# Optimization experiments

Hardware: AMD Instinct MI355X
Metric: run time of the kernel (lower is better)

The kernel has to match this reference:

```python
import jax, jax.numpy as jnp
import numpy as np

S, L, V, E, H, LBL, CH = 4096, 16, 100000, 256, 512, 64, 4


def setup_inputs() -> dict:
    key = jax.random.key(0)
    ks = jax.random.split(key, 10)
    sc = lambda k, shp, fan: (jax.random.normal(k, shp, jnp.float32) / np.sqrt(fan)).astype(jnp.float32)
    return {
        "sentence": jax.random.randint(ks[0], (S,), 0, V, dtype=jnp.int32),
        "chars": jax.random.normal(ks[1], (S, L), dtype=jnp.float32),
        "char_lens": jax.random.randint(ks[2], (S,), 1, L + 1, dtype=jnp.int32),
        "emb": jax.random.normal(ks[3], (V, E), dtype=jnp.float32),
        "W_ih_c": sc(ks[4], (4 * CH, 1), 1),
        "W_hh_c": sc(ks[5], (4 * CH, CH), CH),
        "b_ih_c": jnp.zeros((4 * CH,), jnp.float32),
        "b_hh_c": jnp.zeros((4 * CH,), jnp.float32),
        "W_ih_w": sc(ks[6], (4 * H, E + CH), E + CH),
        "W_hh_w": sc(ks[7], (4 * H, H), H),
        "b_ih_w": jnp.zeros((4 * H,), jnp.float32),
        "b_hh_w": jnp.zeros((4 * H,), jnp.float32),
        "W_out": sc(ks[8], (LBL, H), H),
        "b_out": jnp.zeros((LBL,), jnp.float32),
    }


def _lstm_gates(gates, c):
    i, f, g, o = jnp.split(gates, 4, axis=-1)
    c_new = jax.nn.sigmoid(f) * c + jax.nn.sigmoid(i) * jnp.tanh(g)
    h_new = jax.nn.sigmoid(o) * jnp.tanh(c_new)
    return h_new, c_new


def reference(sentence, chars, char_lens, emb, W_ih_c, W_hh_c, b_ih_c, b_hh_c,
              W_ih_w, W_hh_w, b_ih_w, b_hh_w, W_out, b_out):
    s, l = chars.shape
    # --- char-level LSTM, batched over all words (ragged -> padded + mask) ---
    # input projection: input_size == 1, so gates_x[s, t] = chars[s, t] * W_ih_c[:, 0] + b_ih_c
    gx = chars[:, :, None] * W_ih_c[:, 0] + b_ih_c          # [S, L, 4*CH]
    gx_t = jnp.transpose(gx, (1, 0, 2))                      # [L, S, 4*CH]
    mask = (jnp.arange(l)[:, None] < char_lens[None, :])[:, :, None]  # [L, S, 1]

    def char_step(carry, inp):
        h, c = carry
        g, m = inp
        h_new, c_new = _lstm_gates(g + h @ W_hh_c.T + b_hh_c, c)
        return (jnp.where(m, h_new, h), jnp.where(m, c_new, c)), None

    ch0 = jnp.zeros((s, W_hh_c.shape[1]), chars.dtype)
    (h_char, _), _ = jax.lax.scan(char_step, (ch0, ch0), (gx_t, mask))  # h_char: [S, CH]

    # --- word-level LSTM over the sentence ---
    word_in = jnp.concatenate([emb[sentence], h_char], axis=-1)  # [S, E+CH]
    gx_w = word_in @ W_ih_w.T + b_ih_w                           # [S, 4*H]

    def word_step(carry, g):
        h, c = carry
        h_new, c_new = _lstm_gates(g + h @ W_hh_w.T + b_hh_w, c)
        return (h_new, c_new), h_new

    wh0 = jnp.zeros((W_hh_w.shape[1],), chars.dtype)
    _, hs = jax.lax.scan(word_step, (wh0, wh0), gx_w)            # [S, H]

    logits = hs @ W_out.T + b_out                                # [S, LBL]
    return jax.nn.log_softmax(logits, axis=-1)
```

## Files before the change

kernel.cpp:

```cpp
#include <hip/hip_runtime.h>
#include <stdint.h>

#define SLEN 4096
#define CLEN 16
#define EDIM 256
#define HDIM 512
#define CHD  4
#define NLBL 64
#define KIN  260
#define G4H  2048

typedef unsigned long long u64;

__device__ __forceinline__ float sigf(float x){ return 1.0f/(1.0f+__expf(-x)); }
__device__ __forceinline__ float ftanh(float x){
  float e = __expf(2.0f*x);
  return 1.0f - 2.0f/(e+1.0f);
}
#define RLANE(x,i) __uint_as_float(__builtin_amdgcn_readlane(__float_as_uint(x),(i)))

__global__ void k_char_lstm(const float* __restrict__ chars, const int* __restrict__ lens,
                            const float* __restrict__ Wih, const float* __restrict__ Whh,
                            const float* __restrict__ bih, const float* __restrict__ bhh,
                            float* __restrict__ h_char){
  int s = blockIdx.x*blockDim.x + threadIdx.x;
  if (s >= SLEN) return;
  float wih[16], bb[16], whh[16][4];
  #pragma unroll
  for(int r=0;r<16;r++){
    wih[r]=Wih[r]; bb[r]=bih[r]+bhh[r];
    #pragma unroll
    for(int k=0;k<4;k++) whh[r][k]=Whh[r*4+k];
  }
  float x[16];
  #pragma unroll
  for(int i=0;i<4;i++){
    float4 v = *(const float4*)&chars[s*CLEN + 4*i];
    x[4*i+0]=v.x; x[4*i+1]=v.y; x[4*i+2]=v.z; x[4*i+3]=v.w;
  }
  float h[4]={0,0,0,0}, c[4]={0,0,0,0};
  int len = lens[s];
  #pragma unroll 1
  for(int t=0;t<CLEN;t++){
    float g[16];
    #pragma unroll
    for(int r=0;r<16;r++){
      float a = fmaf(x[t], wih[r], bb[r]);
      #pragma unroll
      for(int k=0;k<4;k++) a = fmaf(h[k], whh[r][k], a);
      g[r]=a;
    }
    bool m = t < len;
    #pragma unroll
    for(int j=0;j<4;j++){
      float ig=sigf(g[j]), fg=sigf(g[4+j]), gg=ftanh(g[8+j]), og=sigf(g[12+j]);
      float cn = fg*c[j] + ig*gg;
      float hn = og*ftanh(cn);
      if(m){ c[j]=cn; h[j]=hn; }
    }
  }
  #pragma unroll
  for(int j=0;j<4;j++) h_char[s*CHD+j]=h[j];
}

__global__ void k_gather(const int* __restrict__ sent, const float* __restrict__ emb,
                         const float* __restrict__ h_char, float* __restrict__ win){
  int s = blockIdx.x; int l = threadIdx.x;
  int row = sent[s];
  float4 v = *(const float4*)&emb[(size_t)row*EDIM + 4*l];
  *(float4*)&win[(size_t)s*KIN + 4*l] = v;
  if (l < CHD) win[(size_t)s*KIN + EDIM + l] = h_char[s*CHD + l];
}

#define BK 20
__global__ __launch_bounds__(256) void k_gemm_gx(const float* __restrict__ win,
                          const float* __restrict__ Wihw, float* __restrict__ gx){
  __shared__ float As[BK][68];
  __shared__ float Bs[BK][68];
  int s0 = blockIdx.x*64, n0 = blockIdx.y*64;
  int tid = threadIdx.x;
  int tm = tid>>4, tn = tid&15;
  float acc[4][4] = {};
  for(int k0=0;k0<KIN;k0+=BK){
    __syncthreads();
    #pragma unroll
    for(int i=0;i<5;i++){
      int e = tid + i*256;
      int m = e/BK, kk = e - m*BK;
      As[kk][m] = win[(size_t)(s0+m)*KIN + k0+kk];
      Bs[kk][m] = Wihw[(size_t)(n0+m)*KIN + k0+kk];
    }
    __syncthreads();
    #pragma unroll
    for(int kk=0;kk<BK;kk++){
      float4 a4 = *(const float4*)&As[kk][tm*4];
      float4 b4 = *(const float4*)&Bs[kk][tn*4];
      float av[4]={a4.x,a4.y,a4.z,a4.w};
      float bv[4]={b4.x,b4.y,b4.z,b4.w};
      #pragma unroll
      for(int i=0;i<4;i++)
        #pragma unroll
        for(int j=0;j<4;j++)
          acc[i][j] = fmaf(av[i], bv[j], acc[i][j]);
    }
  }
  #pragma unroll
  for(int i=0;i<4;i++){
    float4 o; o.x=acc[i][0]; o.y=acc[i][1]; o.z=acc[i][2]; o.w=acc[i][3];
    *(float4*)&gx[(size_t)(s0+tm*4+i)*G4H + n0 + tn*4] = o;
  }
}

__global__ __launch_bounds__(512) void k_word_lstm(const float* __restrict__ gx,
    const float* __restrict__ Whh, const float* __restrict__ bih, const float* __restrict__ bhh,
    u64* __restrict__ comm, float* __restrict__ hs){
  __shared__ float pbuf[2][8][64];
  const int tid = threadIdx.x;
  const int g   = blockIdx.x;
  const int w   = tid>>6;
  const int l   = tid&63;
  const int R   = (l>>4)*HDIM + g*16 + (l&15);
  const int gi  = g*16 + tid;
  float4 w4[16];
  #pragma unroll
  for(int i=0;i<16;i++) w4[i] = *(const float4*)&Whh[(size_t)R*HDIM + w*64 + 4*i];
  float cst = 0.f;
  float bsum[4], gxv[4];
  if (tid<16){
    #pragma unroll
    for(int q=0;q<4;q++){
      bsum[q] = bih[q*HDIM + gi] + bhh[q*HDIM + gi];
      gxv[q]  = gx[(size_t)0*G4H + q*HDIM + gi];
    }
  }

  #pragma unroll 1
  for(int t=0;t<SLEN;t++){
    const int par = t&1;
    float hv = 0.f;
    if (t>0){
      const u64* slot = &comm[(size_t)par*HDIM + w*64 + l];
      u64 v;
      do { v = __hip_atomic_load(slot, __ATOMIC_RELAXED, __HIP_MEMORY_SCOPE_AGENT); }
      while ((unsigned)(v>>32) != (unsigned)t);
      union{unsigned u; float f;} cv; cv.u = (unsigned)v; hv = cv.f;
    }
    float a0=0.f, a1=0.f, a2=0.f, a3=0.f;
    #pragma unroll
    for(int i=0;i<16;i++){
      float4 wv = w4[i];
      a0 = fmaf(wv.x, RLANE(hv,4*i+0), a0);
      a1 = fmaf(wv.y, RLANE(hv,4*i+1), a1);
      a2 = fmaf(wv.z, RLANE(hv,4*i+2), a2);
      a3 = fmaf(wv.w, RLANE(hv,4*i+3), a3);
    }
    pbuf[par][w][l] = (a0+a1)+(a2+a3);
    __syncthreads();
    if (tid < 64){
      const float* pb = &pbuf[par][0][0];
      float s = pb[tid];
      #pragma unroll
      for(int q=1;q<8;q++) s += pb[q*64 + tid];
      float a16 = __shfl_down(s,16);
      float a32 = __shfl_down(s,32);
      float a48 = __shfl_down(s,48);
      if (tid<16){
        float gi_ = s   + gxv[0] + bsum[0];
        float gf_ = a16 + gxv[1] + bsum[1];
        float gg_ = a32 + gxv[2] + bsum[2];
        float go_ = a48 + gxv[3] + bsum[3];
        float cn = sigf(gf_)*cst + sigf(gi_)*ftanh(gg_);
        float hn = sigf(go_)*ftanh(cn);
        cst = cn;
        union{float f; unsigned u;} hb; hb.f = hn;
        u64 pk = ((u64)(unsigned)(t+1)<<32) | (u64)hb.u;
        __hip_atomic_store(&comm[(size_t)((t+1)&1)*HDIM + gi], pk,
                           __ATOMIC_RELAXED, __HIP_MEMORY_SCOPE_AGENT);
        hs[(size_t)t*HDIM + gi] = hn;
        if (t+1 < SLEN){
          #pragma unroll
          for(int q=0;q<4;q++) gxv[q] = gx[(size_t)(t+1)*G4H + q*HDIM + gi];
        }
      }
    }
  }
}

__global__ __launch_bounds__(256) void k_out(const float* __restrict__ hs,
        const float* __restrict__ Wout, const float* __restrict__ bout,
        float* __restrict__ out){
  __shared__ float hsub[HDIM];
  __shared__ float lg[NLBL];
  int s = blockIdx.x, tid = threadIdx.x;
  hsub[tid]     = hs[(size_t)s*HDIM + tid];
  hsub[tid+256] = hs[(size_t)s*HDIM + tid + 256];
  __syncthreads();
  int l = tid>>2, q = tid&3;
  float a = 0.f;
  const float* wrp = &Wout[(size_t)l*HDIM + q*128];
  const float* hr = &hsub[q*128];
  #pragma unroll 8
  for(int i=0;i<128;i++) a = fmaf(hr[i], wrp[i], a);
  a += __shfl_xor(a,1);
  a += __shfl_xor(a,2);
  if (q==0) lg[l] = a + bout[l];
  __syncthreads();
  if (tid < NLBL){
    float x = lg[tid];
    float mx = x;
    #pragma unroll
    for(int m=32;m>=1;m>>=1) mx = fmaxf(mx, __shfl_xor(mx,m));
    float ex = __expf(x-mx);
    float sm = ex;
    #pragma unroll
    for(int m=32;m>=1;m>>=1) sm += __shfl_xor(sm,m);
    out[(size_t)s*NLBL + tid] = x - mx - __logf(sm);
  }
}

extern "C" void kernel_launch(void* const* d_in, const int* in_sizes, int n_in,
                              void* d_out, int out_size, void* d_ws, size_t ws_size,
                              hipStream_t stream){
  const int*   sent  = (const int*)d_in[0];
  const float* chars = (const float*)d_in[1];
  const int*   lens  = (const int*)d_in[2];
  const float* emb   = (const float*)d_in[3];
  const float* Wihc  = (const float*)d_in[4];
  const float* Whhc  = (const float*)d_in[5];
  const float* bihc  = (const float*)d_in[6];
  const float* bhhc  = (const float*)d_in[7];
  const float* Wihw  = (const float*)d_in[8];
  const float* Whhw  = (const float*)d_in[9];
  const float* bihw  = (const float*)d_in[10];
  const float* bhhw  = (const float*)d_in[11];
  const float* Wout  = (const float*)d_in[12];
  const float* bout  = (const float*)d_in[13];
  float* out = (float*)d_out;

  float* h_char = (float*)d_ws;
  float* win    = h_char + 16384;
  float* gx     = win + (size_t)SLEN*KIN;
  float* hs     = gx + (size_t)SLEN*G4H;
  u64*   comm   = (u64*)(hs + (size_t)SLEN*HDIM);

  k_char_lstm<<<SLEN/256, 256, 0, stream>>>(chars,lens,Wihc,Whhc,bihc,bhhc,h_char);
  k_gather<<<SLEN, 64, 0, stream>>>(sent,emb,h_char,win);
  k_gemm_gx<<<dim3(SLEN/64, G4H/64), 256, 0, stream>>>(win,Wihw,gx);
  k_word_lstm<<<HDIM/16, 512, 0, stream>>>(gx,Whhw,bihw,bhhw,comm,hs);
  k_out<<<SLEN, 256, 0, stream>>>(hs,Wout,bout,out);
}
```

Before: 6.105 ms.

## Co-locate word-LSTM workgroups on one XCD and exchange state through its L2

```diff
diff --git a/kernel.cpp b/kernel.cpp
--- a/kernel.cpp
+++ b/kernel.cpp
@@ -18,6 +18,17 @@
   return 1.0f - 2.0f/(e+1.0f);
 }
 #define RLANE(x,i) __uint_as_float(__builtin_amdgcn_readlane(__float_as_uint(x),(i)))
+
+__device__ __forceinline__ u64 l2_load_u64(const u64* p){
+  u64 v;
+  asm volatile("global_load_dwordx2 %0, %1, off sc0\n\ts_waitcnt vmcnt(0)"
+               : "=v"(v) : "v"(p) : "memory");
+  return v;
+}
+__device__ __forceinline__ void l2_store_u64(u64* p, u64 v){
+  asm volatile("global_store_dwordx2 %0, %1, off sc0"
+               :: "v"(p), "v"(v) : "memory");
+}
 
 __global__ void k_char_lstm(const float* __restrict__ chars, const int* __restrict__ lens,
                             const float* __restrict__ Wih, const float* __restrict__ Whh,
@@ -113,10 +124,31 @@
 
 __global__ __launch_bounds__(512) void k_word_lstm(const float* __restrict__ gx,
     const float* __restrict__ Whh, const float* __restrict__ bih, const float* __restrict__ bhh,
-    u64* __restrict__ comm, float* __restrict__ hs){
+    unsigned* __restrict__ ctrl, u64* __restrict__ comm_fast, u64* __restrict__ comm_slow,
+    float* __restrict__ hs){
   __shared__ float pbuf[2][8][64];
+  __shared__ int s_g;
   const int tid = threadIdx.x;
-  const int g   = blockIdx.x;
+  if (tid==0){
+    unsigned xcd;
+    asm volatile("s_getreg_b32 %0, hwreg(HW_REG_XCC_ID)" : "=s"(xcd));
+    xcd &= 7u;
+    unsigned slot = __hip_atomic_fetch_add(&ctrl[xcd], 1u,
+                        __ATOMIC_RELAXED, __HIP_MEMORY_SCOPE_AGENT);
+    if (slot == 31u){
+      unsigned exp = 0u;
+      __hip_atomic_compare_exchange_strong(&ctrl[8], &exp, xcd+1u,
+          __ATOMIC_RELAXED, __ATOMIC_RELAXED, __HIP_MEMORY_SCOPE_AGENT);
+    }
+    unsigned wn;
+    do { wn = __hip_atomic_load(&ctrl[8], __ATOMIC_RELAXED, __HIP_MEMORY_SCOPE_AGENT); }
+    while (wn == 0u);
+    s_g = (slot < 32u && wn == xcd+1u) ? (int)slot : -1;
+  }
+  __syncthreads();
+  const int g = s_g;
+  if (g < 0) return;
+
   const int w   = tid>>6;
   const int l   = tid&63;
   const int R   = (l>>4)*HDIM + g*16 + (l&15);
@@ -139,10 +171,18 @@
     const int par = t&1;
     float hv = 0.f;
     if (t>0){
-      const u64* slot = &comm[(size_t)par*HDIM + w*64 + l];
-      u64 v;
-      do { v = __hip_atomic_load(slot, __ATOMIC_RELAXED, __HIP_MEMORY_SCOPE_AGENT); }
-      while ((unsigned)(v>>32) != (unsigned)t);
+      const u64* fs = &comm_fast[(size_t)par*HDIM + w*64 + l];
+      u64 v = 0; bool got = false;
+      #pragma unroll 1
+      for(int p=0;p<4;p++){
+        v = l2_load_u64(fs);
+        if ((unsigned)(v>>32) == (unsigned)t){ got = true; break; }
+      }
+      if (!got){
+        const u64* ss = &comm_slow[(size_t)par*HDIM + w*64 + l];
+        do { v = __hip_atomic_load(ss, __ATOMIC_RELAXED, __HIP_MEMORY_SCOPE_AGENT); }
+        while ((unsigned)(v>>32) != (unsigned)t);
+      }
       union{unsigned u; float f;} cv; cv.u = (unsigned)v; hv = cv.f;
     }
     float a0=0.f, a1=0.f, a2=0.f, a3=0.f;
@@ -174,7 +214,9 @@
         cst = cn;
         union{float f; unsigned u;} hb; hb.f = hn;
         u64 pk = ((u64)(unsigned)(t+1)<<32) | (u64)hb.u;
-        __hip_atomic_store(&comm[(size_t)((t+1)&1)*HDIM + gi], pk,
+        const size_t off = (size_t)((t+1)&1)*HDIM + gi;
+        l2_store_u64(&comm_fast[off], pk);
+        __hip_atomic_store(&comm_slow[off], pk,
                            __ATOMIC_RELAXED, __HIP_MEMORY_SCOPE_AGENT);
         hs[(size_t)t*HDIM + gi] = hn;
         if (t+1 < SLEN){
@@ -237,15 +279,18 @@
   const float* bout  = (const float*)d_in[13];
   float* out = (float*)d_out;
 
-  float* h_char = (float*)d_ws;
+  unsigned* ctrl = (unsigned*)d_ws;
+  float* h_char = (float*)d_ws + 32;
   float* win    = h_char + 16384;
   float* gx     = win + (size_t)SLEN*KIN;
   float* hs     = gx + (size_t)SLEN*G4H;
-  u64*   comm   = (u64*)(hs + (size_t)SLEN*HDIM);
-
+  u64*   comm_fast = (u64*)(hs + (size_t)SLEN*HDIM);
+  u64*   comm_slow = comm_fast + 2*HDIM;
+
+  hipMemsetAsync(ctrl, 0, 64, stream);
   k_char_lstm<<<SLEN/256, 256, 0, stream>>>(chars,lens,Wihc,Whhc,bihc,bhhc,h_char);
   k_gather<<<SLEN, 64, 0, stream>>>(sent,emb,h_char,win);
   k_gemm_gx<<<dim3(SLEN/64, G4H/64), 256, 0, stream>>>(win,Wihw,gx);
-  k_word_lstm<<<HDIM/16, 512, 0, stream>>>(gx,Whhw,bihw,bhhw,comm,hs);
+  k_word_lstm<<<256, 512, 0, stream>>>(gx,Whhw,bihw,bhhw,ctrl,comm_fast,comm_slow,hs);
   k_out<<<SLEN, 256, 0, stream>>>(hs,Wout,bout,out);
 }
```

After: 7.697 ms. 26.1% more time.
